# Kernel tuning notes

Hardware: AMD Instinct MI355X
Metric: run time of the kernel (lower is better)

The kernel has to match this reference:

```python
import jax, jax.numpy as jnp
import numpy as np

B, C_IN, M = 512, 200, 128  # M = n_nodes + 1 (zero-pad slot 0)
N3 = 3 * (M - 1)            # 3 gather indices (node,left,right) per node
H1, H2, F = 512, 512, 256   # conv channel sizes, F = feature_dim


def tree_conv(data, idx, w, b):
    # data: [B, C, M]; idx: [B, 3N] int indices into M; w: [O, C, 3]; b: [O]
    gathered = jnp.take_along_axis(data, idx[:, None, :].astype(jnp.int32), axis=2)  # [B, C, 3N]
    g = gathered.reshape(data.shape[0], data.shape[1], -1, 3)  # [B, C, N, 3]
    out = jnp.einsum('bcnk,ock->bon', g, w) + b[None, :, None]  # Conv1d(k=3, stride=3)
    zero = jnp.zeros((data.shape[0], w.shape[0], 1), out.dtype)  # re-attach pad slot 0
    return jnp.concatenate([zero, out], axis=2)  # [B, O, M]


def tree_layer_norm(data):
    # per-tree normalization over (channel, node) dims; torch.std is unbiased (ddof=1)
    mean = jnp.mean(data, axis=(1, 2), keepdims=True)
    std = jnp.std(data, axis=(1, 2), keepdims=True, ddof=1)
    return (data - mean) / (std + 1e-5)


def setup_inputs() -> dict:
    key = jax.random.key(0)
    ks = jax.random.split(key, 16)
    s = 0.05
    inp = {
        'trees': jax.random.normal(ks[0], (B, C_IN, M), jnp.float32),
        'indexes': jax.random.randint(ks[1], (B, N3, 1), 0, M, jnp.int32),
        # plan_embedding_nn conv stack
        'w1': jax.random.normal(ks[2], (H1, C_IN, 3), jnp.float32) * s,
        'b1': jnp.zeros((H1,), jnp.float32),
        'w2': jax.random.normal(ks[3], (H2, H1, 3), jnp.float32) * s,
        'b2': jnp.zeros((H2,), jnp.float32),
        'w3': jax.random.normal(ks[4], (F, H2, 3), jnp.float32) * s,
        'b3': jnp.zeros((F,), jnp.float32),
        # gate_nn: Linear(F, F//2) ReLU Linear(F//2, 1)
        'gw1': jax.random.normal(ks[5], (F // 2, F), jnp.float32) * s,
        'gb1': jnp.zeros((F // 2,), jnp.float32),
        'gw2': jax.random.normal(ks[6], (1, F // 2), jnp.float32) * s,
        'gb2': jnp.zeros((1,), jnp.float32),
        'rw1': jax.random.normal(ks[7], (128, 2 * F), jnp.float32) * s,
        'rb1': jnp.zeros((128,), jnp.float32),
        'rw2': jax.random.normal(ks[8], (64, 128), jnp.float32) * s,
        'rb2': jnp.zeros((64,), jnp.float32),
        'rw3': jax.random.normal(ks[9], (1, 64), jnp.float32) * s,
        'rb3': jnp.zeros((1,), jnp.float32),
    }
    return inp


def reference(trees, indexes, w1, b1, w2, b2, w3, b3, gw1, gb1, gw2, gb2,
              rw1, rb1, rw2, rb2, rw3, rb3):
    idx = indexes[..., 0]  # [B, 3N]
    x = jax.nn.relu(tree_layer_norm(tree_conv(trees, idx, w1, b1)))
    x = jax.nn.relu(tree_layer_norm(tree_conv(x, idx, w2, b2)))
    emb = tree_conv(x, idx, w3, b3)            # [B, F, M]
    et = jnp.transpose(emb, (0, 2, 1))         # [B, M, F]
    # GlobalAttention pooling: segments are the equal-size per-plan node sets,
    # so segment-softmax == softmax over the node axis.
    gate = jax.nn.relu(jnp.einsum('bmf,hf->bmh', et, gw1) + gb1)
    gate = jnp.einsum('bmh,oh->bmo', gate, gw2) + gb2   # [B, M, 1]
    attn = jax.nn.softmax(gate, axis=1)
    pool = jnp.sum(attn * et, axis=1)          # [B, F]
    root = et[:, 1, :]                         # slot 1 = root node
    combined = jnp.concatenate([root, pool], axis=1)  # [B, 2F]
    h = jax.nn.relu(combined @ rw1.T + rb1)
    h = jax.nn.relu(h @ rw2.T + rb2)
    out = h @ rw3.T + rb3                      # [B, 1]
    return out, combined
```

## Files before the change

### kernel.cpp

```cpp
#include <hip/hip_runtime.h>
#include <stdint.h>

#define DI __device__ __forceinline__

static constexpr int B_   = 512;
static constexpr int N3_  = 381;

typedef short bf16x8 __attribute__((ext_vector_type(8)));
typedef float f32x4  __attribute__((ext_vector_type(4)));

DI float bf2f(uint32_t u) { union { uint32_t i; float f; } v; v.i = u << 16; return v.f; }
DI uint16_t f2bf(float f) {
  union { float f; uint32_t i; } v; v.f = f;
  uint32_t x = v.i;
  return (uint16_t)((x + 0x7fffu + ((x >> 16) & 1u)) >> 16);
}
DI void unpack8(uint4 u, float* v) {
  v[0] = bf2f(u.x & 0xffffu); v[1] = bf2f(u.x >> 16);
  v[2] = bf2f(u.y & 0xffffu); v[3] = bf2f(u.y >> 16);
  v[4] = bf2f(u.z & 0xffffu); v[5] = bf2f(u.z >> 16);
  v[6] = bf2f(u.w & 0xffffu); v[7] = bf2f(u.w >> 16);
}

DI void ldsload16(const uint16_t* g, uint16_t* l) {
  __builtin_amdgcn_global_load_lds((const __attribute__((address_space(1))) void*)g,
                                   (__attribute__((address_space(3))) void*)l,
                                   16, 0, 0);
}

struct PrepArgs {
  const void* trees; const void* w1; const void* w2; const void* w3; const void* gw1;
  const void* b1; const void* b2; const void* b3; const void* gb1;
  const void* gw2; const void* gb2;
  const void* rw1; const void* rb1; const void* rw2; const void* rb2;
  const void* rw3; const void* rb3;
  uint16_t* treesT; uint16_t* W1b; uint16_t* W2b; uint16_t* W3b; uint16_t* GW1b;
  float* b1f; float* b2f; float* b3f; float* gb1f; float* gw2f; float* gb2f;
  float* rw1f; float* rb1f; float* rw2f; float* rb2f; float* rw3f; float* rb3f;
  int* flagp; float* statsAcc;
};

static constexpr int PREP_TRANS_END = 3584;
static constexpr int PREP_W1_END    = 3840;
static constexpr int PREP_W2_END    = 4352;
static constexpr int PREP_W3_END    = 4608;
static constexpr int PREP_GW1_END   = 4640;
static constexpr int PREP_F32_END   = 4672;

DI void wcvt_range(const void* src, uint16_t* dst, int O, int C, int Cpad,
                   int isf32, int idx, int nb) {
  int Kpad = 3 * Cpad;
  int n = O * Kpad;
  int stride = nb * 256;
  for (int i = idx * 256 + (int)threadIdx.x; i < n; i += stride) {
    int o = i / Kpad, e = i - o * Kpad;
    int reg = e / Cpad, c = e - reg * Cpad;
    uint16_t v = 0;
    if (c < C) {
      int s = (o * C + c) * 3 + reg;
      v = isf32 ? f2bf(((const float*)src)[s]) : ((const uint16_t*)src)[s];
    }
    dst[i] = v;
  }
}

DI void fcvt_range(const void* src, float* dst, int n, int isf32, int idx, int nb) {
  int stride = nb * 256;
  for (int i = idx * 256 + (int)threadIdx.x; i < n; i += stride)
    dst[i] = isf32 ? ((const float*)src)[i] : bf2f(((const uint16_t*)src)[i]);
}

__global__ __launch_bounds__(256)
void prep_kernel(PrepArgs a) {
  __shared__ int cnt;
  __shared__ uint16_t sX[32][130];

  const int id = blockIdx.x;
  const int tx = threadIdx.x;

  if (tx == 0) cnt = 0;
  __syncthreads();
  {
    const uint16_t* t16 = (const uint16_t*)a.trees;
    int local = 0;
    #pragma unroll
    for (int q = 0; q < 2; q++) {
      uint16_t u = t16[tx * 2 + q];
      int ex = (u >> 7) & 0xff;
      if (ex >= 110 && ex <= 133) local++;
    }
    atomicAdd(&cnt, local);
  }
  __syncthreads();
  const int isf32 = (cnt >= 450) ? 0 : 1;

  if (id == 0) {
    if (tx == 0) *a.flagp = isf32;
    #pragma unroll
    for (int q = 0; q < 8; q++) a.statsAcc[q * 256 + tx] = 0.f;
  }

  if (id < PREP_TRANS_END) {
    const int b = id / 7, c0 = (id % 7) * 32;
    const int cn = min(32, 200 - c0);
    if (isf32) {
      const float* src = (const float*)a.trees + ((size_t)b * 200 + c0) * 128;
      for (int t = tx; t < cn * 128; t += 256) {
        int c = t >> 7, m = t & 127;
        sX[c][m] = f2bf(src[c * 128 + m]);
      }
    } else {
      const uint32_t* src = (const uint32_t*)((const uint16_t*)a.trees + ((size_t)b * 200 + c0) * 128);
      for (int t = tx; t < cn * 64; t += 256) {
        int c = t >> 6, p = t & 63;
        ((uint32_t*)&sX[c][0])[p] = src[c * 64 + p];
      }
    }
    __syncthreads();
    uint32_t* out = (uint32_t*)(a.treesT + (size_t)b * 129 * 256 + c0);
    for (int p = tx; p < 129 * 16; p += 256) {
      int m = p >> 4, u = p & 15;
      int c = u * 2;
      uint32_t v = 0;
      if (m < 128) {
        uint16_t lo = (c     < cn) ? sX[c][m]     : (uint16_t)0;
        uint16_t hi = (c + 1 < cn) ? sX[c + 1][m] : (uint16_t)0;
        v = (uint32_t)lo | ((uint32_t)hi << 16);
      }
      out[(size_t)m * 128 + u] = v;
    }
  } else if (id < PREP_W1_END) {
    wcvt_range(a.w1, a.W1b, 512, 200, 256, isf32, id - PREP_TRANS_END, PREP_W1_END - PREP_TRANS_END);
  } else if (id < PREP_W2_END) {
    wcvt_range(a.w2, a.W2b, 512, 512, 512, isf32, id - PREP_W1_END, PREP_W2_END - PREP_W1_END);
  } else if (id < PREP_W3_END) {
    wcvt_range(a.w3, a.W3b, 256, 512, 512, isf32, id - PREP_W2_END, PREP_W3_END - PREP_W2_END);
  } else if (id < PREP_GW1_END) {
    int idx = id - PREP_W3_END, nb = PREP_GW1_END - PREP_W3_END;
    int stride = nb * 256;
    for (int i = idx * 256 + tx; i < 128 * 256; i += stride)
      a.GW1b[i] = isf32 ? f2bf(((const float*)a.gw1)[i]) : ((const uint16_t*)a.gw1)[i];
  } else {
    int idx = id - PREP_GW1_END, nb = PREP_F32_END - PREP_GW1_END;
    fcvt_range(a.rw1, a.rw1f, 128 * 512, isf32, idx, nb);
    fcvt_range(a.rw2, a.rw2f, 64 * 128, isf32, idx, nb);
    if (idx == 0) {
      fcvt_range(a.b1, a.b1f, 512, isf32, 0, 1);
      fcvt_range(a.b2, a.b2f, 512, isf32, 0, 1);
      fcvt_range(a.b3, a.b3f, 256, isf32, 0, 1);
      fcvt_range(a.gb1, a.gb1f, 128, isf32, 0, 1);
      fcvt_range(a.gw2, a.gw2f, 128, isf32, 0, 1);
      fcvt_range(a.gb2, a.gb2f, 1, isf32, 0, 1);
      fcvt_range(a.rb1, a.rb1f, 128, isf32, 0, 1);
      fcvt_range(a.rb2, a.rb2f, 64, isf32, 0, 1);
      fcvt_range(a.rw3, a.rw3f, 64, isf32, 0, 1);
      fcvt_range(a.rb3, a.rb3f, 1, isf32, 0, 1);
    }
  }
}

__global__ __launch_bounds__(256, 2)
void gemm_kernel(const uint16_t* __restrict__ A,
                 const uint16_t* __restrict__ xT,
                 const int* __restrict__ idxg,
                 const float* __restrict__ bias,
                 uint16_t* __restrict__ Y,
                 int nO, int Cpad, int outRS,
                 float* __restrict__ statsAcc) {
  __shared__ __align__(16) uint16_t sA[256 * 64];
  __shared__ __align__(16) uint16_t sB[128 * 64];
  __shared__ float sBias[256];
  __shared__ int sIdx[384];
  __shared__ float2 sRed[256];

  const int id   = blockIdx.x;
  const int xcd  = id & 7;
  const int rest = id >> 3;
  const int ot   = rest % nO;
  const int b    = (rest / nO) * 8 + xcd;
  const int obase = ot * 256;
  const int O     = nO * 256;

  const int tx    = threadIdx.x;
  const int wave  = tx >> 6, lane = tx & 63;
  const int wj    = wave & 1, wo = wave >> 1;
  const int Kpad  = 3 * Cpad;

  for (int t = tx; t < N3_; t += 256) sIdx[t] = idxg[(size_t)b * N3_ + t];
  sBias[tx] = bias[obase + tx];
  __syncthreads();

  const uint16_t* Abase = A + (size_t)obase * Kpad;
  const uint16_t* Bbase = xT + (size_t)b * 129 * Cpad;

  const int srow = lane >> 3;
  const int schk = lane & 7;
  const int lm = lane & 15;
  const int kg = lane >> 4;

  f32x4 zero4 = {0.f, 0.f, 0.f, 0.f};
  f32x4 acc[4][8];
  #pragma unroll
  for (int i = 0; i < 4; i++)
    #pragma unroll
    for (int j = 0; j < 8; j++) acc[i][j] = zero4;

  for (int reg = 0; reg < 3; reg++) {
    int ridx[4];
    #pragma unroll
    for (int i = 0; i < 4; i++) {
      int r = i * 32 + wave * 8 + srow;
      ridx[i] = (r == 0) ? 128 : sIdx[3 * (r - 1) + reg];
    }
    for (int co = 0; co < Cpad; co += 64) {
      __syncthreads();
      #pragma unroll
      for (int i = 0; i < 8; i++) {
        int r  = i * 32 + wave * 8 + srow;
        int ca = schk ^ (r & 7);
        ldsload16(Abase + (size_t)r * Kpad + reg * Cpad + co + ca * 8,
                  &sA[(i * 32 + wave * 8) * 64]);
      }
      #pragma unroll
      for (int i = 0; i < 4; i++) {
        int r  = i * 32 + wave * 8 + srow;
        int ca = schk ^ (r & 7);
        ldsload16(Bbase + (size_t)ridx[i] * Cpad + co + ca * 8,
                  &sB[(i * 32 + wave * 8) * 64]);
      }
      __syncthreads();
      #pragma unroll
      for (int s = 0; s < 2; s++) {
        bf16x8 xv[4], wv[8];
        #pragma unroll
        for (int f = 0; f < 4; f++) {
          int rj = wj * 64 + f * 16 + lm;
          int cj = (s * 4 + kg) ^ (rj & 7);
          xv[f] = *(const bf16x8*)&sB[rj * 64 + cj * 8];
        }
        #pragma unroll
        for (int f = 0; f < 8; f++) {
          int ro = wo * 128 + f * 16 + lm;
          int cw = (s * 4 + kg) ^ (ro & 7);
          wv[f] = *(const bf16x8*)&sA[ro * 64 + cw * 8];
        }
        #pragma unroll
        for (int fj = 0; fj < 4; fj++)
          #pragma unroll
          for (int fo = 0; fo < 8; fo++)
            acc[fj][fo] = __builtin_amdgcn_mfma_f32_16x16x32_bf16(xv[fj], wv[fo], acc[fj][fo], 0, 0, 0);
      }
    }
  }

  float s1 = 0.f, s2 = 0.f;
  #pragma unroll
  for (int fj = 0; fj < 4; fj++) {
    #pragma unroll
    for (int fo = 0; fo < 8; fo++) {
      int olocal = wo * 128 + fo * 16 + lm;
      float bo = sBias[olocal];
      #pragma unroll
      for (int r = 0; r < 4; r++) {
        int j = wj * 64 + fj * 16 + kg * 4 + r;
        float v = acc[fj][fo][r] + bo;
        if (j == 0) v = 0.f;
        s1 += v; s2 += v * v;
        Y[((size_t)b * outRS + j) * O + obase + olocal] = f2bf(v);
      }
    }
  }

  if (statsAcc) {
    sRed[tx] = make_float2(s1, s2);
    __syncthreads();
    for (int s = 128; s > 0; s >>= 1) {
      if (tx < s) { sRed[tx].x += sRed[tx + s].x; sRed[tx].y += sRed[tx + s].y; }
      __syncthreads();
    }
    if (tx == 0) {
      atomicAdd(&statsAcc[b * 2],     sRed[0].x);
      atomicAdd(&statsAcc[b * 2 + 1], sRed[0].y);
    }
  }
}

__global__ __launch_bounds__(256)
void ln_relu_kernel(uint16_t* __restrict__ y, const float* __restrict__ statsAcc,
                    float count) {
  const int total = B_ * 129 * 64;
  int stride = gridDim.x * blockDim.x;
  for (int i = blockIdx.x * blockDim.x + threadIdx.x; i < total; i += stride) {
    int rowG = i >> 6;
    int b = rowG / 129;
    int r = rowG - b * 129;
    uint4 out;
    if (r == 128) {
      out = make_uint4(0, 0, 0, 0);
    } else {
      float s = statsAcc[b * 2], ss = statsAcc[b * 2 + 1];
      float mean = s / count;
      float var = fmaxf((ss - s * s / count) / (count - 1.0f), 0.f);
      float scale = 1.0f / (sqrtf(var) + 1e-5f);
      uint4 u = ((const uint4*)y)[i];
      float v[8]; unpack8(u, v);
      uint32_t rr[4];
      #pragma unroll
      for (int k = 0; k < 4; k++) {
        float a  = fmaxf((v[2 * k]     - mean) * scale, 0.f);
        float bb = fmaxf((v[2 * k + 1] - mean) * scale, 0.f);
        rr[k] = (uint32_t)f2bf(a) | ((uint32_t)f2bf(bb) << 16);
      }
      out = make_uint4(rr[0], rr[1], rr[2], rr[3]);
    }
    ((uint4*)y)[i] = out;
  }
}

__global__ __launch_bounds__(256)
void gate_kernel(const uint16_t* __restrict__ emb,
                 const uint16_t* __restrict__ gw1b,
                 const float* __restrict__ gb1,
                 const float* __restrict__ gw2, const float* __restrict__ gb2,
                 const float* __restrict__ rw1, const float* __restrict__ rb1,
                 const float* __restrict__ rw2, const float* __restrict__ rb2,
                 const float* __restrict__ rw3, const float* __restrict__ rb3,
                 void* __restrict__ dout, const int* __restrict__ flag) {
  __shared__ __align__(16) uint16_t sEmb[128 * 64];
  __shared__ float sRed[4][128];
  __shared__ float sSm[128];
  __shared__ float sAttn[128];
  __shared__ float sPool4[4 * 256];
  __shared__ __align__(16) float sC[512];
  __shared__ __align__(16) float sH1[128];
  __shared__ float sH2[64];

  const int b = blockIdx.x;
  const int tx = threadIdx.x;
  const int wave = tx >> 6, lane = tx & 63;
  const int lm = lane & 15, kg = lane >> 4;
  const int srow = lane >> 3, schk = lane & 7;
  const int h0 = wave * 32;
  const uint16_t* embB = emb + (size_t)b * 128 * 256;

  f32x4 zero4 = {0.f, 0.f, 0.f, 0.f};
  f32x4 acc[2][8];
  #pragma unroll
  for (int i = 0; i < 2; i++)
    #pragma unroll
    for (int t = 0; t < 8; t++) acc[i][t] = zero4;

  for (int kc = 0; kc < 256; kc += 64) {
    __syncthreads();
    #pragma unroll
    for (int i = 0; i < 4; i++) {
      int r  = wave * 8 + i * 32 + srow;
      int ca = schk ^ (r & 7);
      ldsload16(embB + (size_t)r * 256 + kc + ca * 8, &sEmb[(wave * 8 + i * 32) * 64]);
    }
    __syncthreads();
    #pragma unroll
    for (int s = 0; s < 2; s++) {
      bf16x8 a0 = *(const bf16x8*)(gw1b + (size_t)(h0 + lm) * 256 + kc + s * 32 + kg * 8);
      bf16x8 a1 = *(const bf16x8*)(gw1b + (size_t)(h0 + 16 + lm) * 256 + kc + s * 32 + kg * 8);
      #pragma unroll
      for (int t = 0; t < 8; t++) {
        int rn = t * 16 + lm;
        int cn = (s * 4 + kg) ^ (rn & 7);
        bf16x8 bv = *(const bf16x8*)&sEmb[rn * 64 + cn * 8];
        acc[0][t] = __builtin_amdgcn_mfma_f32_16x16x32_bf16(a0, bv, acc[0][t], 0, 0, 0);
        acc[1][t] = __builtin_amdgcn_mfma_f32_16x16x32_bf16(a1, bv, acc[1][t], 0, 0, 0);
      }
    }
  }

  float gb[2][4], gv[2][4];
  #pragma unroll
  for (int ht = 0; ht < 2; ht++)
    #pragma unroll
    for (int r = 0; r < 4; r++) {
      int h = h0 + ht * 16 + kg * 4 + r;
      gb[ht][r] = gb1[h]; gv[ht][r] = gw2[h];
    }
  float p[8];
  #pragma unroll
  for (int t = 0; t < 8; t++) {
    float s = 0.f;
    #pragma unroll
    for (int ht = 0; ht < 2; ht++)
      #pragma unroll
      for (int r = 0; r < 4; r++)
        s += fmaxf(acc[ht][t][r] + gb[ht][r], 0.f) * gv[ht][r];
    s += __shfl_xor(s, 16);
    s += __shfl_xor(s, 32);
    p[t] = s;
  }
  if (lane < 16) {
    #pragma unroll
    for (int t = 0; t < 8; t++) sRed[wave][t * 16 + lane] = p[t];
  }
  __syncthreads();

  float e = 0.f;
  if (tx < 128) {
    float v = sRed[0][tx] + sRed[1][tx] + sRed[2][tx] + sRed[3][tx] + gb2[0];
    sSm[tx] = v;
    sAttn[tx] = v;
  }
  __syncthreads();
  for (int s = 64; s > 0; s >>= 1) {
    if (tx < s) sSm[tx] = fmaxf(sSm[tx], sSm[tx + s]);
    __syncthreads();
  }
  float mx = sSm[0];
  __syncthreads();
  if (tx < 128) { e = expf(sAttn[tx] - mx); sSm[tx] = e; }
  __syncthreads();
  for (int s = 64; s > 0; s >>= 1) {
    if (tx < s) sSm[tx] += sSm[tx + s];
    __syncthreads();
  }
  float denom = sSm[0];
  __syncthreads();
  if (tx < 128) sAttn[tx] = e / denom;
  __syncthreads();

  float pl00 = 0.f, pl01 = 0.f, pl10 = 0.f, pl11 = 0.f;
  const uint32_t* base = (const uint32_t*)embB;
  const int mw = wave * 32;
  for (int mi = 0; mi < 32; mi++) {
    float a = sAttn[mw + mi];
    uint32_t u0 = base[(size_t)(mw + mi) * 128 + lane];
    uint32_t u1 = base[(size_t)(mw + mi) * 128 + 64 + lane];
    pl00 = fmaf(a, bf2f(u0 & 0xffffu), pl00);
    pl01 = fmaf(a, bf2f(u0 >> 16),     pl01);
    pl10 = fmaf(a, bf2f(u1 & 0xffffu), pl10);
    pl11 = fmaf(a, bf2f(u1 >> 16),     pl11);
  }
  sPool4[wave * 256 + lane * 2]           = pl00;
  sPool4[wave * 256 + lane * 2 + 1]       = pl01;
  sPool4[wave * 256 + 128 + lane * 2]     = pl10;
  sPool4[wave * 256 + 128 + lane * 2 + 1] = pl11;
  __syncthreads();

  float pool = sPool4[tx] + sPool4[256 + tx] + sPool4[512 + tx] + sPool4[768 + tx];
  float root = bf2f(embB[256 + tx]);
  sC[tx]       = root;
  sC[256 + tx] = pool;

  const int isf32 = (*flag != 0);
  if (!isf32) {
    uint16_t* o = ((uint16_t*)dout) + 512;
    o[b * 512 + tx]       = f2bf(root);
    o[b * 512 + 256 + tx] = f2bf(pool);
  } else {
    float* o = ((float*)dout) + 512;
    o[b * 512 + tx]       = root;
    o[b * 512 + 256 + tx] = pool;
  }
  __syncthreads();

  if (tx < 128) {
    float a = rb1[tx];
    const float4* wr = (const float4*)(rw1 + (size_t)tx * 512);
    for (int i = 0; i < 128; i++) {
      float4 w4 = wr[i];
      float4 c4 = *(const float4*)&sC[i * 4];
      a = fmaf(w4.x, c4.x, a); a = fmaf(w4.y, c4.y, a);
      a = fmaf(w4.z, c4.z, a); a = fmaf(w4.w, c4.w, a);
    }
    sH1[tx] = fmaxf(a, 0.f);
  }
  __syncthreads();
  if (tx < 64) {
    float a2 = rb2[tx];
    const float4* wr2 = (const float4*)(rw2 + (size_t)tx * 128);
    for (int i = 0; i < 32; i++) {
      float4 w4 = wr2[i];
      float4 h4 = *(const float4*)&sH1[i * 4];
      a2 = fmaf(w4.x, h4.x, a2); a2 = fmaf(w4.y, h4.y, a2);
      a2 = fmaf(w4.z, h4.z, a2); a2 = fmaf(w4.w, h4.w, a2);
    }
    sH2[tx] = fmaxf(a2, 0.f);
  }
  __syncthreads();
  if (tx < 64) {
    float pv = sH2[tx] * rw3[tx];
    for (int off = 32; off > 0; off >>= 1) pv += __shfl_down(pv, off);
    if (tx == 0) {
      float o = pv + rb3[0];
      if (!isf32) ((uint16_t*)dout)[b] = f2bf(o);
      else        ((float*)dout)[b]    = o;
    }
  }
}

extern "C" void kernel_launch(void* const* d_in, const int* in_sizes, int n_in,
                              void* d_out, int out_size, void* d_ws, size_t ws_size,
                              hipStream_t stream) {
  const void* trees   = d_in[0];
  const int*  indexes = (const int*)d_in[1];

  char* ws = (char*)d_ws;
  size_t off = 0;
  auto alloc = [&](size_t bytes) -> char* {
    char* p = ws + off;
    off += (bytes + 255) & ~(size_t)255;
    return p;
  };

  int*   flagp    = (int*)alloc(256);
  float* statsAcc = (float*)alloc(4 * B_ * sizeof(float));
  float* b1f = (float*)alloc(512 * 4);
  float* b2f = (float*)alloc(512 * 4);
  float* b3f = (float*)alloc(256 * 4);
  float* gb1f = (float*)alloc(128 * 4);
  float* gw2f = (float*)alloc(128 * 4);
  float* gb2f = (float*)alloc(4);
  float* rw1f = (float*)alloc(128 * 512 * 4);
  float* rb1f = (float*)alloc(128 * 4);
  float* rw2f = (float*)alloc(64 * 128 * 4);
  float* rb2f = (float*)alloc(64 * 4);
  float* rw3f = (float*)alloc(64 * 4);
  float* rb3f = (float*)alloc(4);
  uint16_t* W1b  = (uint16_t*)alloc((size_t)512 * 768 * 2);
  uint16_t* W2b  = (uint16_t*)alloc((size_t)512 * 1536 * 2);
  uint16_t* W3b  = (uint16_t*)alloc((size_t)256 * 1536 * 2);
  uint16_t* GW1b = (uint16_t*)alloc((size_t)128 * 256 * 2);
  uint16_t* bufA = (uint16_t*)alloc((size_t)B_ * 129 * 512 * 2);
  uint16_t* bufB = (uint16_t*)alloc((size_t)B_ * 129 * 512 * 2);

  uint16_t* treesT = bufB;
  uint16_t* y1T    = bufA;
  uint16_t* y2T    = bufB;
  uint16_t* yT3    = bufA;

  PrepArgs pa;
  pa.trees = trees;
  pa.w1 = d_in[2];  pa.b1 = d_in[3];
  pa.w2 = d_in[4];  pa.b2 = d_in[5];
  pa.w3 = d_in[6];  pa.b3 = d_in[7];
  pa.gw1 = d_in[8]; pa.gb1 = d_in[9];
  pa.gw2 = d_in[10]; pa.gb2 = d_in[11];
  pa.rw1 = d_in[12]; pa.rb1 = d_in[13];
  pa.rw2 = d_in[14]; pa.rb2 = d_in[15];
  pa.rw3 = d_in[16]; pa.rb3 = d_in[17];
  pa.treesT = treesT; pa.W1b = W1b; pa.W2b = W2b; pa.W3b = W3b; pa.GW1b = GW1b;
  pa.b1f = b1f; pa.b2f = b2f; pa.b3f = b3f; pa.gb1f = gb1f; pa.gw2f = gw2f; pa.gb2f = gb2f;
  pa.rw1f = rw1f; pa.rb1f = rb1f; pa.rw2f = rw2f; pa.rb2f = rb2f; pa.rw3f = rw3f; pa.rb3f = rb3f;
  pa.flagp = flagp; pa.statsAcc = statsAcc;

  prep_kernel<<<PREP_F32_END, 256, 0, stream>>>(pa);

  gemm_kernel<<<2 * B_, 256, 0, stream>>>(
      W1b, treesT, indexes, b1f, y1T, 2, 256, 129, statsAcc);
  ln_relu_kernel<<<2048, 256, 0, stream>>>(y1T, statsAcc, 65536.f);

  gemm_kernel<<<2 * B_, 256, 0, stream>>>(
      W2b, y1T, indexes, b2f, y2T, 2, 512, 129, statsAcc + 2 * B_);
  ln_relu_kernel<<<2048, 256, 0, stream>>>(y2T, statsAcc + 2 * B_, 65536.f);

  gemm_kernel<<<B_, 256, 0, stream>>>(
      W3b, y2T, indexes, b3f, yT3, 1, 512, 128, nullptr);

  gate_kernel<<<B_, 256, 0, stream>>>(yT3, GW1b, gb1f, gw2f, gb2f,
                                      rw1f, rb1f, rw2f, rb2f, rw3f, rb3f,
                                      d_out, flagp);

  (void)in_sizes; (void)n_in; (void)out_size; (void)ws_size;
}
```

Baseline: 411.8 us.

## Fuse third tree conv GEMM into gate/pooling tail kernel via LDS

```diff
diff --git a/kernel.cpp b/kernel.cpp
--- a/kernel.cpp
+++ b/kernel.cpp
@@ -271,38 +271,36 @@
     }
   }
 
-  if (statsAcc) {
-    sRed[tx] = make_float2(s1, s2);
+  sRed[tx] = make_float2(s1, s2);
+  __syncthreads();
+  for (int s = 128; s > 0; s >>= 1) {
+    if (tx < s) { sRed[tx].x += sRed[tx + s].x; sRed[tx].y += sRed[tx + s].y; }
     __syncthreads();
-    for (int s = 128; s > 0; s >>= 1) {
-      if (tx < s) { sRed[tx].x += sRed[tx + s].x; sRed[tx].y += sRed[tx + s].y; }
-      __syncthreads();
-    }
-    if (tx == 0) {
-      atomicAdd(&statsAcc[b * 2],     sRed[0].x);
-      atomicAdd(&statsAcc[b * 2 + 1], sRed[0].y);
-    }
+  }
+  if (tx == 0) {
+    atomicAdd(&statsAcc[b * 2],     sRed[0].x);
+    atomicAdd(&statsAcc[b * 2 + 1], sRed[0].y);
   }
 }
 
 __global__ __launch_bounds__(256)
 void ln_relu_kernel(uint16_t* __restrict__ y, const float* __restrict__ statsAcc,
                     float count) {
-  const int total = B_ * 129 * 64;
-  int stride = gridDim.x * blockDim.x;
-  for (int i = blockIdx.x * blockDim.x + threadIdx.x; i < total; i += stride) {
-    int rowG = i >> 6;
-    int b = rowG / 129;
-    int r = rowG - b * 129;
+  const int b    = blockIdx.x >> 2;
+  const int part = blockIdx.x & 3;
+  float s = statsAcc[b * 2], ss = statsAcc[b * 2 + 1];
+  float mean = s / count;
+  float var = fmaxf((ss - s * s / count) / (count - 1.0f), 0.f);
+  float scale = 1.0f / (sqrtf(var) + 1e-5f);
+
+  uint4* yb = (uint4*)y + (size_t)b * 8256;
+  for (int i = part * 2064 + threadIdx.x; i < (part + 1) * 2064; i += 256) {
+    int r = i >> 6;
     uint4 out;
     if (r == 128) {
       out = make_uint4(0, 0, 0, 0);
     } else {
-      float s = statsAcc[b * 2], ss = statsAcc[b * 2 + 1];
-      float mean = s / count;
-      float var = fmaxf((ss - s * s / count) / (count - 1.0f), 0.f);
-      float scale = 1.0f / (sqrtf(var) + 1e-5f);
-      uint4 u = ((const uint4*)y)[i];
+      uint4 u = yb[i];
       float v[8]; unpack8(u, v);
       uint32_t rr[4];
       #pragma unroll
@@ -313,12 +311,15 @@
       }
       out = make_uint4(rr[0], rr[1], rr[2], rr[3]);
     }
-    ((uint4*)y)[i] = out;
-  }
-}
-
-__global__ __launch_bounds__(256)
-void gate_kernel(const uint16_t* __restrict__ emb,
+    yb[i] = out;
+  }
+}
+
+__global__ __launch_bounds__(256, 2)
+void tail_kernel(const uint16_t* __restrict__ W3,
+                 const uint16_t* __restrict__ xT,
+                 const int* __restrict__ idxg,
+                 const float* __restrict__ b3,
                  const uint16_t* __restrict__ gw1b,
                  const float* __restrict__ gb1,
                  const float* __restrict__ gw2, const float* __restrict__ gb2,
@@ -326,8 +327,10 @@
                  const float* __restrict__ rw2, const float* __restrict__ rb2,
                  const float* __restrict__ rw3, const float* __restrict__ rb3,
                  void* __restrict__ dout, const int* __restrict__ flag) {
-  __shared__ __align__(16) uint16_t sEmb[128 * 64];
-  __shared__ float sRed[4][128];
+  __shared__ __align__(16) uint16_t sEmbF[4][128][64];
+  __shared__ float sBias[256];
+  __shared__ int sIdx[384];
+  __shared__ float sRedG[4][128];
   __shared__ float sSm[128];
   __shared__ float sAttn[128];
   __shared__ float sPool4[4 * 256];
@@ -335,41 +338,118 @@
   __shared__ __align__(16) float sH1[128];
   __shared__ float sH2[64];
 
-  const int b = blockIdx.x;
+  uint16_t* sA = &sEmbF[0][0][0];
+  uint16_t* sB = sA + 256 * 64;
+
+  const int b  = blockIdx.x;
   const int tx = threadIdx.x;
   const int wave = tx >> 6, lane = tx & 63;
+  const int wj = wave & 1, wo = wave >> 1;
   const int lm = lane & 15, kg = lane >> 4;
   const int srow = lane >> 3, schk = lane & 7;
+  const int Kpad = 1536, Cpad = 512;
+
+  for (int t = tx; t < N3_; t += 256) sIdx[t] = idxg[(size_t)b * N3_ + t];
+  sBias[tx] = b3[tx];
+  __syncthreads();
+
+  const uint16_t* Bbase = xT + (size_t)b * 129 * Cpad;
+
+  f32x4 zero4 = {0.f, 0.f, 0.f, 0.f};
+  f32x4 acc[4][8];
+  #pragma unroll
+  for (int i = 0; i < 4; i++)
+    #pragma unroll
+    for (int j = 0; j < 8; j++) acc[i][j] = zero4;
+
+  for (int reg = 0; reg < 3; reg++) {
+    int ridx[4];
+    #pragma unroll
+    for (int i = 0; i < 4; i++) {
+      int r = i * 32 + wave * 8 + srow;
+      ridx[i] = (r == 0) ? 128 : sIdx[3 * (r - 1) + reg];
+    }
+    for (int co = 0; co < Cpad; co += 64) {
+      __syncthreads();
+      #pragma unroll
+      for (int i = 0; i < 8; i++) {
+        int r  = i * 32 + wave * 8 + srow;
+        int ca = schk ^ (r & 7);
+        ldsload16(W3 + (size_t)r * Kpad + reg * Cpad + co + ca * 8,
+                  &sA[(i * 32 + wave * 8) * 64]);
+      }
+      #pragma unroll
+      for (int i = 0; i < 4; i++) {
+        int r  = i * 32 + wave * 8 + srow;
+        int ca = schk ^ (r & 7);
+        ldsload16(Bbase + (size_t)ridx[i] * Cpad + co + ca * 8,
+                  &sB[(i * 32 + wave * 8) * 64]);
+      }
+      __syncthreads();
+      #pragma unroll
+      for (int s = 0; s < 2; s++) {
+        bf16x8 xv[4], wv[8];
+        #pragma unroll
+        for (int f = 0; f < 4; f++) {
+          int rj = wj * 64 + f * 16 + lm;
+          int cj = (s * 4 + kg) ^ (rj & 7);
+          xv[f] = *(const bf16x8*)&sB[rj * 64 + cj * 8];
+        }
+        #pragma unroll
+        for (int f = 0; f < 8; f++) {
+          int ro = wo * 128 + f * 16 + lm;
+          int cw = (s * 4 + kg) ^ (ro & 7);
+          wv[f] = *(const bf16x8*)&sA[ro * 64 + cw * 8];
+        }
+        #pragma unroll
+        for (int fj = 0; fj < 4; fj++)
+          #pragma unroll
+          for (int fo = 0; fo < 8; fo++)
+            acc[fj][fo] = __builtin_amdgcn_mfma_f32_16x16x32_bf16(xv[fj], wv[fo], acc[fj][fo], 0, 0, 0);
+      }
+    }
+  }
+
+  __syncthreads();
+  #pragma unroll
+  for (int fj = 0; fj < 4; fj++) {
+    #pragma unroll
+    for (int fo = 0; fo < 8; fo++) {
+      int olocal = wo * 128 + fo * 16 + lm;
+      int sec = olocal >> 6, oc = olocal & 63;
+      float bo = sBias[olocal];
+      #pragma unroll
+      for (int r = 0; r < 4; r++) {
+        int j = wj * 64 + fj * 16 + kg * 4 + r;
+        float v = acc[fj][fo][r] + bo;
+        if (j == 0) v = 0.f;
+        int chunk = (oc >> 3) ^ (j & 7);
+        sEmbF[sec][j][chunk * 8 + (oc & 7)] = f2bf(v);
+      }
+    }
+  }
+  __syncthreads();
+
   const int h0 = wave * 32;
-  const uint16_t* embB = emb + (size_t)b * 128 * 256;
-
-  f32x4 zero4 = {0.f, 0.f, 0.f, 0.f};
-  f32x4 acc[2][8];
+  f32x4 acc2[2][8];
   #pragma unroll
   for (int i = 0; i < 2; i++)
     #pragma unroll
-    for (int t = 0; t < 8; t++) acc[i][t] = zero4;
-
-  for (int kc = 0; kc < 256; kc += 64) {
-    __syncthreads();
-    #pragma unroll
-    for (int i = 0; i < 4; i++) {
-      int r  = wave * 8 + i * 32 + srow;
-      int ca = schk ^ (r & 7);
-      ldsload16(embB + (size_t)r * 256 + kc + ca * 8, &sEmb[(wave * 8 + i * 32) * 64]);
-    }
-    __syncthreads();
+    for (int t = 0; t < 8; t++) acc2[i][t] = zero4;
+
+  #pragma unroll
+  for (int s4 = 0; s4 < 4; s4++) {
     #pragma unroll
     for (int s = 0; s < 2; s++) {
-      bf16x8 a0 = *(const bf16x8*)(gw1b + (size_t)(h0 + lm) * 256 + kc + s * 32 + kg * 8);
-      bf16x8 a1 = *(const bf16x8*)(gw1b + (size_t)(h0 + 16 + lm) * 256 + kc + s * 32 + kg * 8);
+      bf16x8 a0 = *(const bf16x8*)(gw1b + (size_t)(h0 + lm) * 256 + s4 * 64 + s * 32 + kg * 8);
+      bf16x8 a1 = *(const bf16x8*)(gw1b + (size_t)(h0 + 16 + lm) * 256 + s4 * 64 + s * 32 + kg * 8);
       #pragma unroll
       for (int t = 0; t < 8; t++) {
         int rn = t * 16 + lm;
         int cn = (s * 4 + kg) ^ (rn & 7);
-        bf16x8 bv = *(const bf16x8*)&sEmb[rn * 64 + cn * 8];
-        acc[0][t] = __builtin_amdgcn_mfma_f32_16x16x32_bf16(a0, bv, acc[0][t], 0, 0, 0);
-        acc[1][t] = __builtin_amdgcn_mfma_f32_16x16x32_bf16(a1, bv, acc[1][t], 0, 0, 0);
+        bf16x8 bv = *(const bf16x8*)&sEmbF[s4][rn][cn * 8];
+        acc2[0][t] = __builtin_amdgcn_mfma_f32_16x16x32_bf16(a0, bv, acc2[0][t], 0, 0, 0);
+        acc2[1][t] = __builtin_amdgcn_mfma_f32_16x16x32_bf16(a1, bv, acc2[1][t], 0, 0, 0);
       }
     }
   }
@@ -390,20 +470,20 @@
     for (int ht = 0; ht < 2; ht++)
       #pragma unroll
       for (int r = 0; r < 4; r++)
-        s += fmaxf(acc[ht][t][r] + gb[ht][r], 0.f) * gv[ht][r];
+        s += fmaxf(acc2[ht][t][r] + gb[ht][r], 0.f) * gv[ht][r];
     s += __shfl_xor(s, 16);
     s += __shfl_xor(s, 32);
     p[t] = s;
   }
   if (lane < 16) {
     #pragma unroll
-    for (int t = 0; t < 8; t++) sRed[wave][t * 16 + lane] = p[t];
+    for (int t = 0; t < 8; t++) sRedG[wave][t * 16 + lane] = p[t];
   }
   __syncthreads();
 
   float e = 0.f;
   if (tx < 128) {
-    float v = sRed[0][tx] + sRed[1][tx] + sRed[2][tx] + sRed[3][tx] + gb2[0];
+    float v = sRedG[0][tx] + sRedG[1][tx] + sRedG[2][tx] + sRedG[3][tx] + gb2[0];
     sSm[tx] = v;
     sAttn[tx] = v;
   }
@@ -425,26 +505,37 @@
   if (tx < 128) sAttn[tx] = e / denom;
   __syncthreads();
 
-  float pl00 = 0.f, pl01 = 0.f, pl10 = 0.f, pl11 = 0.f;
-  const uint32_t* base = (const uint32_t*)embB;
-  const int mw = wave * 32;
-  for (int mi = 0; mi < 32; mi++) {
-    float a = sAttn[mw + mi];
-    uint32_t u0 = base[(size_t)(mw + mi) * 128 + lane];
-    uint32_t u1 = base[(size_t)(mw + mi) * 128 + 64 + lane];
-    pl00 = fmaf(a, bf2f(u0 & 0xffffu), pl00);
-    pl01 = fmaf(a, bf2f(u0 >> 16),     pl01);
-    pl10 = fmaf(a, bf2f(u1 & 0xffffu), pl10);
-    pl11 = fmaf(a, bf2f(u1 >> 16),     pl11);
-  }
-  sPool4[wave * 256 + lane * 2]           = pl00;
-  sPool4[wave * 256 + lane * 2 + 1]       = pl01;
-  sPool4[wave * 256 + 128 + lane * 2]     = pl10;
-  sPool4[wave * 256 + 128 + lane * 2 + 1] = pl11;
+  {
+    const int f0 = 2 * lane;
+    const int sec0 = f0 >> 6, oc0 = f0 & 63;
+    const int sec2 = sec0 + 2;
+    float pl00 = 0.f, pl01 = 0.f, pl10 = 0.f, pl11 = 0.f;
+    const int mw = wave * 32;
+    for (int mi = 0; mi < 32; mi++) {
+      int m = mw + mi;
+      float a = sAttn[m];
+      int idx = ((oc0 >> 3) ^ (m & 7)) * 8 + (oc0 & 7);
+      uint32_t u0 = *(const uint32_t*)&sEmbF[sec0][m][idx];
+      uint32_t u1 = *(const uint32_t*)&sEmbF[sec2][m][idx];
+      pl00 = fmaf(a, bf2f(u0 & 0xffffu), pl00);
+      pl01 = fmaf(a, bf2f(u0 >> 16),     pl01);
+      pl10 = fmaf(a, bf2f(u1 & 0xffffu), pl10);
+      pl11 = fmaf(a, bf2f(u1 >> 16),     pl11);
+    }
+    sPool4[wave * 256 + lane * 2]           = pl00;
+    sPool4[wave * 256 + lane * 2 + 1]       = pl01;
+    sPool4[wave * 256 + 128 + lane * 2]     = pl10;
+    sPool4[wave * 256 + 128 + lane * 2 + 1] = pl11;
+  }
   __syncthreads();
 
   float pool = sPool4[tx] + sPool4[256 + tx] + sPool4[512 + tx] + sPool4[768 + tx];
-  float root = bf2f(embB[256 + tx]);
+  float root;
+  {
+    int sec = tx >> 6, oc = tx & 63;
+    int idx = ((oc >> 3) ^ 1) * 8 + (oc & 7);
+    root = bf2f(sEmbF[sec][1][idx]);
+  }
   sC[tx]       = root;
   sC[256 + tx] = pool;
 
@@ -533,7 +624,6 @@
   uint16_t* treesT = bufB;
   uint16_t* y1T    = bufA;
   uint16_t* y2T    = bufB;
-  uint16_t* yT3    = bufA;
 
   PrepArgs pa;
   pa.trees = trees;
@@ -554,16 +644,14 @@
 
   gemm_kernel<<<2 * B_, 256, 0, stream>>>(
       W1b, treesT, indexes, b1f, y1T, 2, 256, 129, statsAcc);
-  ln_relu_kernel<<<2048, 256, 0, stream>>>(y1T, statsAcc, 65536.f);
+  ln_relu_kernel<<<4 * B_, 256, 0, stream>>>(y1T, statsAcc, 65536.f);
 
   gemm_kernel<<<2 * B_, 256, 0, stream>>>(
       W2b, y1T, indexes, b2f, y2T, 2, 512, 129, statsAcc + 2 * B_);
-  ln_relu_kernel<<<2048, 256, 0, stream>>>(y2T, statsAcc + 2 * B_, 65536.f);
-
-  gemm_kernel<<<B_, 256, 0, stream>>>(
-      W3b, y2T, indexes, b3f, yT3, 1, 512, 128, nullptr);
-
-  gate_kernel<<<B_, 256, 0, stream>>>(yT3, GW1b, gb1f, gw2f, gb2f,
+  ln_relu_kernel<<<4 * B_, 256, 0, stream>>>(y2T, statsAcc + 2 * B_, 65536.f);
+
+  tail_kernel<<<B_, 256, 0, stream>>>(W3b, y2T, indexes, b3f,
+                                      GW1b, gb1f, gw2f, gb2f,
                                       rw1f, rb1f, rw2f, rb2f, rw3f, rb3f,
                                       d_out, flagp);
 
```

Result: faster. 386.1 us (-6.2%).
